# Performance work log

Measured on AMD Instinct MI355X. Metric: run time of the kernel, lower is better.

## Reference

```python
import jax, jax.numpy as jnp
import numpy as np

DT = 0.05
N_STEPS = 3
DAMP = 0.5
C2 = 1.0  # wave_speed^2


def _shift(u, k):
    # causal shift along T (axis=1): prepend k zeros, drop last k
    T = u.shape[1]
    return jnp.pad(u, ((0, 0), (k, 0), (0, 0)))[:, :T, :]


def dx(u):
    return u - _shift(u, 1)


def dxx(u):
    return u - 2.0 * _shift(u, 1) + _shift(u, 2)


def dxxx(u):
    return u - 3.0 * _shift(u, 1) + 3.0 * _shift(u, 2) - _shift(u, 3)


def dxxxx(u):
    return u - 4.0 * _shift(u, 1) + 6.0 * _shift(u, 2) - 4.0 * _shift(u, 3) + _shift(u, 4)


def _rk4_second_order(u0, rhs, dt, n_steps):
    # state (u, v), u_t = v, v_t = rhs(u, v); zero initial velocity
    u, v = u0, jnp.zeros_like(u0)
    for _ in range(n_steps):
        k1u, k1v = v, rhs(u, v)
        k2u, k2v = v + 0.5 * dt * k1v, rhs(u + 0.5 * dt * k1u, v + 0.5 * dt * k1v)
        k3u, k3v = v + 0.5 * dt * k2v, rhs(u + 0.5 * dt * k2u, v + 0.5 * dt * k2v)
        k4u, k4v = v + dt * k3v, rhs(u + dt * k3u, v + dt * k3v)
        u = u + (dt / 6.0) * (k1u + 2.0 * k2u + 2.0 * k3u + k4u)
        v = v + (dt / 6.0) * (k1v + 2.0 * k2v + 2.0 * k3v + k4v)
    return u


def _rk4_first_order(u0, rhs, dt, n_steps):
    u = u0
    for _ in range(n_steps):
        k1 = rhs(u)
        k2 = rhs(u + 0.5 * dt * k1)
        k3 = rhs(u + 0.5 * dt * k2)
        k4 = rhs(u + dt * k3)
        u = u + (dt / 6.0) * (k1 + 2.0 * k2 + 2.0 * k3 + k4)
    return u


def sine_gordon(u0):
    rhs = lambda u, v: C2 * dxx(u) - jnp.sin(u) - DAMP * v
    return _rk4_second_order(u0, rhs, DT, N_STEPS)


def kdv(u0):
    rhs = lambda u: -6.0 * u * dx(u) - dxxx(u) - DAMP * u
    return _rk4_first_order(u0, rhs, DT * 0.5, N_STEPS)


def heimburg_jackson(u0):
    rhs = lambda u, v: dx((1.0 + u + u * u) * dx(u)) - dxxxx(u) - DAMP * v
    return _rk4_second_order(u0, rhs, DT * 0.5, N_STEPS)


def setup_inputs() -> dict:
    key = jax.random.key(0)
    kx, kw = jax.random.split(key)
    B, T, D = 4, 4096, 1024
    x = jax.random.normal(kx, (B, T, D), dtype=jnp.float32)
    solver_mix = jnp.ones((3,), dtype=jnp.float32) / 3.0
    W = jax.random.normal(kw, (D, D), dtype=jnp.float32) * (1.0 / np.sqrt(D))
    b = jnp.zeros((D,), dtype=jnp.float32)
    return {"x": x, "solver_mix": solver_mix, "W": W, "b": b}


def reference(x, solver_mix, W, b):
    x_field = jnp.tanh(x) * 2.0
    w = jax.nn.softmax(solver_mix, axis=0)
    evolved = (
        w[0] * sine_gordon(x_field)
        + w[1] * kdv(x_field)
        + w[2] * heimburg_jackson(x_field)
    )
    out = jnp.einsum("btd,ed->bte", evolved, W) + b
    return out
```

## Files before the change

### kernel.cpp

```cpp
#include <hip/hip_runtime.h>
#include <hip/hip_bf16.h>


typedef __bf16 bf16x8 __attribute__((ext_vector_type(8)));
typedef __bf16 bf16x4 __attribute__((ext_vector_type(4)));
typedef float  floatx4 __attribute__((ext_vector_type(4)));

#define T_DIM 4096
#define D_DIM 1024
#define NP    16
#define HALO  48
#define NCH   32
#define TINT  (NCH * NP - HALO)
#define NTT   9

__device__ __forceinline__ float sg_rhs(float c, float m1, float m2, float vv) {
  float dxx = fmaf(-2.f, m1, c) + m2;
  return dxx - __sinf(c) - 0.5f * vv;
}
__device__ __forceinline__ float kdv_rhs(float c, float m1, float m2, float m3) {
  float dxu = c - m1;
  float dx3 = fmaf(-3.f, m1, c) + fmaf(3.f, m2, -m3);
  return fmaf(-6.f * c, dxu, -dx3 - 0.5f * c);
}
__device__ __forceinline__ float hj_rhs(float c, float m1, float m2, float m3,
                                        float m4, float vv) {
  float gi = (fmaf(c, c, c) + 1.f) * (c - m1);
  float gm = (fmaf(m1, m1, m1) + 1.f) * (m1 - m2);
  float d4 = fmaf(-4.f, m3, fmaf(6.f, m2, fmaf(-4.f, m1, c))) + m4;
  return (gi - gm) - d4 - 0.5f * vv;
}

#define AT(F, i) (((i) >= 0) ? F[(i)] : hl[4 + (i)])
#define XCHG(F) do { \
    hl[0] = __shfl_up(F[NP - 4], 1, 32); \
    hl[1] = __shfl_up(F[NP - 3], 1, 32); \
    hl[2] = __shfl_up(F[NP - 2], 1, 32); \
    hl[3] = __shfl_up(F[NP - 1], 1, 32); \
  } while (0)

__global__ __launch_bounds__(256, 2)
void pde_kernel(const float* __restrict__ x, const float* __restrict__ mix,
                __bf16* __restrict__ evout) {
  const int tid  = threadIdx.x;
  const int tr   = tid & 31;
  const int dcol = tid >> 5;
  const int yq   = blockIdx.y >> 3;
  const int yr   = blockIdx.y & 7;
  const int d    = (yr * 16 + yq) * 8 + dcol;
  const int b    = blockIdx.z;
  const int t0   = blockIdx.x * TINT;
  const int tb   = t0 - HALO + tr * NP;

  float s0 = mix[0], s1 = mix[1], s2 = mix[2];
  float mxv = fmaxf(s0, fmaxf(s1, s2));
  float e0 = __expf(s0 - mxv), e1 = __expf(s1 - mxv), e2 = __expf(s2 - mxv);
  float inv = 1.f / (e0 + e1 + e2);
  float w0 = e0 * inv, w1 = e1 * inv, w2 = e2 * inv;

  const float* xp = x + ((size_t)b * T_DIM) * D_DIM + d;

  float u0[NP], u[NP], v[NP], ut[NP], vt[NP], au[NP], av[NP], ev[NP], hl[4];

  #pragma unroll
  for (int j = 0; j < NP; ++j) {
    int t = tb + j;
    float xv = (t >= 0 && t < T_DIM) ? xp[(size_t)t * D_DIM] : 0.f;
    float xc = fminf(fmaxf(xv, -9.f), 9.f);
    float ex = __expf(2.f * xc);
    u0[j] = 2.f - 4.f * __builtin_amdgcn_rcpf(ex + 1.f);
  }

  {
    const float dt = 0.05f, h = 0.025f, w6 = dt * (1.f / 6.f);
    #pragma unroll
    for (int j = 0; j < NP; ++j) { u[j] = u0[j]; v[j] = 0.f; }
    #pragma unroll 1
    for (int s = 0; s < 3; ++s) {
      XCHG(u);
      #pragma unroll
      for (int i = NP - 1; i >= 0; --i) {
        float k = sg_rhs(u[i], AT(u, i - 1), AT(u, i - 2), v[i]);
        au[i] = v[i]; av[i] = k;
        ut[i] = fmaf(h, v[i], u[i]);
        vt[i] = fmaf(h, k, v[i]);
      }
      XCHG(ut);
      #pragma unroll
      for (int i = NP - 1; i >= 0; --i) {
        float k = sg_rhs(ut[i], AT(ut, i - 1), AT(ut, i - 2), vt[i]);
        au[i] = fmaf(2.f, vt[i], au[i]); av[i] = fmaf(2.f, k, av[i]);
        float nu = fmaf(h, vt[i], u[i]);
        vt[i] = fmaf(h, k, v[i]);
        ut[i] = nu;
      }
      XCHG(ut);
      #pragma unroll
      for (int i = NP - 1; i >= 0; --i) {
        float k = sg_rhs(ut[i], AT(ut, i - 1), AT(ut, i - 2), vt[i]);
        au[i] = fmaf(2.f, vt[i], au[i]); av[i] = fmaf(2.f, k, av[i]);
        float nu = fmaf(dt, vt[i], u[i]);
        vt[i] = fmaf(dt, k, v[i]);
        ut[i] = nu;
      }
      XCHG(ut);
      #pragma unroll
      for (int i = NP - 1; i >= 0; --i) {
        float k = sg_rhs(ut[i], AT(ut, i - 1), AT(ut, i - 2), vt[i]);
        au[i] += vt[i]; av[i] += k;
        u[i] = fmaf(w6, au[i], u[i]);
        v[i] = fmaf(w6, av[i], v[i]);
      }
    }
    #pragma unroll
    for (int j = 0; j < NP; ++j) ev[j] = w0 * u[j];
  }

  {
    const float dt = 0.025f, h = 0.0125f, w6 = dt * (1.f / 6.f);
    #pragma unroll
    for (int j = 0; j < NP; ++j) u[j] = u0[j];
    #pragma unroll 1
    for (int s = 0; s < 3; ++s) {
      XCHG(u);
      #pragma unroll
      for (int i = NP - 1; i >= 0; --i) {
        float k = kdv_rhs(u[i], AT(u, i - 1), AT(u, i - 2), AT(u, i - 3));
        au[i] = k;
        ut[i] = fmaf(h, k, u[i]);
      }
      XCHG(ut);
      #pragma unroll
      for (int i = NP - 1; i >= 0; --i) {
        float k = kdv_rhs(ut[i], AT(ut, i - 1), AT(ut, i - 2), AT(ut, i - 3));
        au[i] = fmaf(2.f, k, au[i]);
        ut[i] = fmaf(h, k, u[i]);
      }
      XCHG(ut);
      #pragma unroll
      for (int i = NP - 1; i >= 0; --i) {
        float k = kdv_rhs(ut[i], AT(ut, i - 1), AT(ut, i - 2), AT(ut, i - 3));
        au[i] = fmaf(2.f, k, au[i]);
        ut[i] = fmaf(dt, k, u[i]);
      }
      XCHG(ut);
      #pragma unroll
      for (int i = NP - 1; i >= 0; --i) {
        float k = kdv_rhs(ut[i], AT(ut, i - 1), AT(ut, i - 2), AT(ut, i - 3));
        u[i] = fmaf(w6, au[i] + k, u[i]);
      }
    }
    #pragma unroll
    for (int j = 0; j < NP; ++j) ev[j] = fmaf(w1, u[j], ev[j]);
  }

  {
    const float dt = 0.025f, h = 0.0125f, w6 = dt * (1.f / 6.f);
    #pragma unroll
    for (int j = 0; j < NP; ++j) { u[j] = u0[j]; v[j] = 0.f; }
    #pragma unroll 1
    for (int s = 0; s < 3; ++s) {
      XCHG(u);
      #pragma unroll
      for (int i = NP - 1; i >= 0; --i) {
        float k = hj_rhs(u[i], AT(u, i - 1), AT(u, i - 2), AT(u, i - 3),
                         AT(u, i - 4), v[i]);
        au[i] = v[i]; av[i] = k;
        ut[i] = fmaf(h, v[i], u[i]);
        vt[i] = fmaf(h, k, v[i]);
      }
      XCHG(ut);
      #pragma unroll
      for (int i = NP - 1; i >= 0; --i) {
        float k = hj_rhs(ut[i], AT(ut, i - 1), AT(ut, i - 2), AT(ut, i - 3),
                         AT(ut, i - 4), vt[i]);
        au[i] = fmaf(2.f, vt[i], au[i]); av[i] = fmaf(2.f, k, av[i]);
        float nu = fmaf(h, vt[i], u[i]);
        vt[i] = fmaf(h, k, v[i]);
        ut[i] = nu;
      }
      XCHG(ut);
      #pragma unroll
      for (int i = NP - 1; i >= 0; --i) {
        float k = hj_rhs(ut[i], AT(ut, i - 1), AT(ut, i - 2), AT(ut, i - 3),
                         AT(ut, i - 4), vt[i]);
        au[i] = fmaf(2.f, vt[i], au[i]); av[i] = fmaf(2.f, k, av[i]);
        float nu = fmaf(dt, vt[i], u[i]);
        vt[i] = fmaf(dt, k, v[i]);
        ut[i] = nu;
      }
      XCHG(ut);
      #pragma unroll
      for (int i = NP - 1; i >= 0; --i) {
        float k = hj_rhs(ut[i], AT(ut, i - 1), AT(ut, i - 2), AT(ut, i - 3),
                         AT(ut, i - 4), vt[i]);
        au[i] += vt[i]; av[i] += k;
        u[i] = fmaf(w6, au[i], u[i]);
        v[i] = fmaf(w6, av[i], v[i]);
      }
    }
    #pragma unroll
    for (int j = 0; j < NP; ++j) ev[j] = fmaf(w2, u[j], ev[j]);
  }

  if (tr >= 3) {
    #pragma unroll
    for (int j = 0; j < NP; ++j) {
      int t = tb + j;
      if (t < T_DIM)
        evout[((size_t)(b * T_DIM + t)) * D_DIM + d] = (__bf16)ev[j];
    }
  }
}

__global__ __launch_bounds__(256)
void convert_w(const float* __restrict__ W, __bf16* __restrict__ Wb) {
  int i = blockIdx.x * 256 + threadIdx.x;
  float4 f = ((const float4*)W)[i];
  bf16x4 o = {(__bf16)f.x, (__bf16)f.y, (__bf16)f.z, (__bf16)f.w};
  ((bf16x4*)Wb)[i] = o;
}

#define GK   1024

__global__ __launch_bounds__(512, 1)
void gemm_kernel(const __bf16* __restrict__ A, const __bf16* __restrict__ Bw,
                 const float* __restrict__ bias, float* __restrict__ out) {
  __shared__ __align__(16) __bf16 As[2][256 * 64];
  __shared__ __align__(16) __bf16 Bs[2][256 * 64];

  const int tid  = threadIdx.x;
  const int lane = tid & 63;
  const int wid  = tid >> 6;
  const int m0   = blockIdx.x * 256;
  const int n0   = blockIdx.y * 256;
  const int wm   = (wid >> 2) * 128;
  const int wn   = (wid & 3) * 64;
  const int l15  = lane & 15;
  const int quad = lane >> 4;

  const int sr  = lane >> 3;
  const int skc = (lane & 7) ^ sr;

  const __bf16* aBase = A  + (size_t)(m0 + wid * 32 + sr) * GK + skc * 8;
  const __bf16* bBase = Bw + (size_t)(n0 + wid * 32 + sr) * GK + skc * 8;

#define STAGE(buf, kt) do {                                                   \
    _Pragma("unroll")                                                         \
    for (int p = 0; p < 4; ++p)                                               \
      __builtin_amdgcn_global_load_lds(                                       \
          (const uint32_t*)(aBase + (size_t)(p * 8) * GK + (kt)),             \
          (uint32_t*)&As[buf][(wid * 32 + p * 8) * 64], 16, 0, 0);            \
    _Pragma("unroll")                                                         \
    for (int p = 0; p < 4; ++p)                                               \
      __builtin_amdgcn_global_load_lds(                                       \
          (const uint32_t*)(bBase + (size_t)(p * 8) * GK + (kt)),             \
          (uint32_t*)&Bs[buf][(wid * 32 + p * 8) * 64], 16, 0, 0);            \
  } while (0)

  floatx4 acc[8][4] = {};

  STAGE(0, 0);
  __syncthreads();

  int cur = 0;
  for (int kt = 64; kt <= GK; kt += 64) {
    if (kt < GK) STAGE(cur ^ 1, kt);
    const __bf16* as = As[cur];
    const __bf16* bs = Bs[cur];
    #pragma unroll
    for (int c = 0; c < 2; ++c) {
      bf16x8 af[8], bfr[4];
      int kcg = c * 4 + quad;
      #pragma unroll
      for (int i = 0; i < 8; ++i) {
        int ra = wm + i * 16 + l15;
        af[i] = *(const bf16x8*)(&as[ra * 64 + ((kcg ^ (ra & 7)) * 8)]);
      }
      #pragma unroll
      for (int j = 0; j < 4; ++j) {
        int rb = wn + j * 16 + l15;
        bfr[j] = *(const bf16x8*)(&bs[rb * 64 + ((kcg ^ (rb & 7)) * 8)]);
      }
      #pragma unroll
      for (int i = 0; i < 8; ++i)
        #pragma unroll
        for (int j = 0; j < 4; ++j)
          acc[i][j] = __builtin_amdgcn_mfma_f32_16x16x32_bf16(
              af[i], bfr[j], acc[i][j], 0, 0, 0);
    }
    __syncthreads();
    cur ^= 1;
  }
#undef STAGE

  #pragma unroll
  for (int j = 0; j < 4; ++j) {
    int n = n0 + wn + j * 16 + l15;
    float bv = bias[n];
    #pragma unroll
    for (int i = 0; i < 8; ++i) {
      int mb = m0 + wm + i * 16 + quad * 4;
      #pragma unroll
      for (int r = 0; r < 4; ++r)
        out[(size_t)(mb + r) * 1024 + n] = acc[i][j][r] + bv;
    }
  }
}

extern "C" void kernel_launch(void* const* d_in, const int* in_sizes, int n_in,
                              void* d_out, int out_size, void* d_ws, size_t ws_size,
                              hipStream_t stream) {
  const float* x    = (const float*)d_in[0];
  const float* mix  = (const float*)d_in[1];
  const float* W    = (const float*)d_in[2];
  const float* bias = (const float*)d_in[3];
  float* out = (float*)d_out;

  __bf16* ev = (__bf16*)d_ws;
  __bf16* Wb = (__bf16*)((char*)d_ws + (size_t)32 * 1024 * 1024);

  convert_w<<<dim3((D_DIM * D_DIM / 4) / 256), 256, 0, stream>>>(W, Wb);
  pde_kernel<<<dim3(NTT, 128, 4), 256, 0, stream>>>(x, mix, ev);
  gemm_kernel<<<dim3(16384 / 256, 1024 / 256), 512, 0, stream>>>(ev, Wb, bias, out);
}
```

Baseline: 324.4 us.

## Halve PDE per-thread points, reuse HJ flux terms, and hand-pipeline GEMM barriers

The PDE kernel now gives each thread 8 time points instead of 16 and spreads a column over a full 64-lane wavefront, with launch bounds raised to allow 4 blocks per CU. This lowers register pressure so occupancy can rise. The Heimburg-Jackson RHS now precomputes the nonlinear flux g once per point and reuses it for neighbours, removing the duplicate gm computation. The GEMM main loop is restructured with explicit vmcnt/lgkmcnt waits, raw s_barriers and a peeled final iteration, so the next tile's global-to-LDS loads can overlap compute. The d-column mapping also changes, which alters memory coalescing and access order.

```diff
diff --git a/kernel.cpp b/kernel.cpp
--- a/kernel.cpp
+++ b/kernel.cpp
@@ -8,9 +8,9 @@
 
 #define T_DIM 4096
 #define D_DIM 1024
-#define NP    16
+#define NP    8
 #define HALO  48
-#define NCH   32
+#define NCH   64
 #define TINT  (NCH * NP - HALO)
 #define NTT   9
 
@@ -23,31 +23,30 @@
   float dx3 = fmaf(-3.f, m1, c) + fmaf(3.f, m2, -m3);
   return fmaf(-6.f * c, dxu, -dx3 - 0.5f * c);
 }
-__device__ __forceinline__ float hj_rhs(float c, float m1, float m2, float m3,
-                                        float m4, float vv) {
-  float gi = (fmaf(c, c, c) + 1.f) * (c - m1);
-  float gm = (fmaf(m1, m1, m1) + 1.f) * (m1 - m2);
+__device__ __forceinline__ float hj_rhs2(float c, float m1, float m2, float m3,
+                                         float m4, float dg, float vv) {
   float d4 = fmaf(-4.f, m3, fmaf(6.f, m2, fmaf(-4.f, m1, c))) + m4;
-  return (gi - gm) - d4 - 0.5f * vv;
+  return (dg - d4) - 0.5f * vv;
+}
+__device__ __forceinline__ float hj_g(float c, float m1) {
+  return (fmaf(c, c, c) + 1.f) * (c - m1);
 }
 
 #define AT(F, i) (((i) >= 0) ? F[(i)] : hl[4 + (i)])
 #define XCHG(F) do { \
-    hl[0] = __shfl_up(F[NP - 4], 1, 32); \
-    hl[1] = __shfl_up(F[NP - 3], 1, 32); \
-    hl[2] = __shfl_up(F[NP - 2], 1, 32); \
-    hl[3] = __shfl_up(F[NP - 1], 1, 32); \
+    hl[0] = __shfl_up(F[NP - 4], 1, 64); \
+    hl[1] = __shfl_up(F[NP - 3], 1, 64); \
+    hl[2] = __shfl_up(F[NP - 2], 1, 64); \
+    hl[3] = __shfl_up(F[NP - 1], 1, 64); \
   } while (0)
 
-__global__ __launch_bounds__(256, 2)
+__global__ __launch_bounds__(256, 4)
 void pde_kernel(const float* __restrict__ x, const float* __restrict__ mix,
                 __bf16* __restrict__ evout) {
   const int tid  = threadIdx.x;
-  const int tr   = tid & 31;
-  const int dcol = tid >> 5;
-  const int yq   = blockIdx.y >> 3;
-  const int yr   = blockIdx.y & 7;
-  const int d    = (yr * 16 + yq) * 8 + dcol;
+  const int tr   = tid & 63;
+  const int dcol = tid >> 6;
+  const int d    = blockIdx.y * 4 + dcol;
   const int b    = blockIdx.z;
   const int t0   = blockIdx.x * TINT;
   const int tb   = t0 - HALO + tr * NP;
@@ -156,54 +155,69 @@
 
   {
     const float dt = 0.025f, h = 0.0125f, w6 = dt * (1.f / 6.f);
+    float g[NP], gB;
+#define HJ_GPRE(SRC) do {                                                  \
+      gB = hj_g(hl[3], hl[2]);                                             \
+      _Pragma("unroll")                                                    \
+      for (int i_ = 0; i_ < NP; ++i_)                                      \
+        g[i_] = hj_g(SRC[i_], AT(SRC, i_ - 1));                            \
+    } while (0)
+#define DG(i) ((i) ? (g[(i) - 1]) : gB)
+
     #pragma unroll
     for (int j = 0; j < NP; ++j) { u[j] = u0[j]; v[j] = 0.f; }
     #pragma unroll 1
     for (int s = 0; s < 3; ++s) {
       XCHG(u);
-      #pragma unroll
-      for (int i = NP - 1; i >= 0; --i) {
-        float k = hj_rhs(u[i], AT(u, i - 1), AT(u, i - 2), AT(u, i - 3),
-                         AT(u, i - 4), v[i]);
+      HJ_GPRE(u);
+      #pragma unroll
+      for (int i = NP - 1; i >= 0; --i) {
+        float k = hj_rhs2(u[i], AT(u, i - 1), AT(u, i - 2), AT(u, i - 3),
+                          AT(u, i - 4), g[i] - DG(i), v[i]);
         au[i] = v[i]; av[i] = k;
         ut[i] = fmaf(h, v[i], u[i]);
         vt[i] = fmaf(h, k, v[i]);
       }
       XCHG(ut);
-      #pragma unroll
-      for (int i = NP - 1; i >= 0; --i) {
-        float k = hj_rhs(ut[i], AT(ut, i - 1), AT(ut, i - 2), AT(ut, i - 3),
-                         AT(ut, i - 4), vt[i]);
+      HJ_GPRE(ut);
+      #pragma unroll
+      for (int i = NP - 1; i >= 0; --i) {
+        float k = hj_rhs2(ut[i], AT(ut, i - 1), AT(ut, i - 2), AT(ut, i - 3),
+                          AT(ut, i - 4), g[i] - DG(i), vt[i]);
         au[i] = fmaf(2.f, vt[i], au[i]); av[i] = fmaf(2.f, k, av[i]);
         float nu = fmaf(h, vt[i], u[i]);
         vt[i] = fmaf(h, k, v[i]);
         ut[i] = nu;
       }
       XCHG(ut);
-      #pragma unroll
-      for (int i = NP - 1; i >= 0; --i) {
-        float k = hj_rhs(ut[i], AT(ut, i - 1), AT(ut, i - 2), AT(ut, i - 3),
-                         AT(ut, i - 4), vt[i]);
+      HJ_GPRE(ut);
+      #pragma unroll
+      for (int i = NP - 1; i >= 0; --i) {
+        float k = hj_rhs2(ut[i], AT(ut, i - 1), AT(ut, i - 2), AT(ut, i - 3),
+                          AT(ut, i - 4), g[i] - DG(i), vt[i]);
         au[i] = fmaf(2.f, vt[i], au[i]); av[i] = fmaf(2.f, k, av[i]);
         float nu = fmaf(dt, vt[i], u[i]);
         vt[i] = fmaf(dt, k, v[i]);
         ut[i] = nu;
       }
       XCHG(ut);
-      #pragma unroll
-      for (int i = NP - 1; i >= 0; --i) {
-        float k = hj_rhs(ut[i], AT(ut, i - 1), AT(ut, i - 2), AT(ut, i - 3),
-                         AT(ut, i - 4), vt[i]);
+      HJ_GPRE(ut);
+      #pragma unroll
+      for (int i = NP - 1; i >= 0; --i) {
+        float k = hj_rhs2(ut[i], AT(ut, i - 1), AT(ut, i - 2), AT(ut, i - 3),
+                          AT(ut, i - 4), g[i] - DG(i), vt[i]);
         au[i] += vt[i]; av[i] += k;
         u[i] = fmaf(w6, au[i], u[i]);
         v[i] = fmaf(w6, av[i], v[i]);
       }
     }
+#undef HJ_GPRE
+#undef DG
     #pragma unroll
     for (int j = 0; j < NP; ++j) ev[j] = fmaf(w2, u[j], ev[j]);
   }
 
-  if (tr >= 3) {
+  if (tr >= HALO / NP) {
     #pragma unroll
     for (int j = 0; j < NP; ++j) {
       int t = tb + j;
@@ -258,41 +272,56 @@
           (uint32_t*)&Bs[buf][(wid * 32 + p * 8) * 64], 16, 0, 0);            \
   } while (0)
 
+#define COMPUTE(buf) do {                                                     \
+    const __bf16* as_ = As[buf];                                              \
+    const __bf16* bs_ = Bs[buf];                                              \
+    _Pragma("unroll")                                                         \
+    for (int c = 0; c < 2; ++c) {                        \
+      bf16x8 af[8], bfr[4];                                                   \
+      int kcg = c * 4 + quad;                  \
+      _Pragma("unroll")                                                       \
+      for (int i = 0; i < 8; ++i) {                                           \
+        int ra = wm + i * 16 + l15;                                           \
+        af[i] = *(const bf16x8*)(&as_[ra * 64 + ((kcg ^ (ra & 7)) * 8)]);     \
+      }                                                                       \
+      _Pragma("unroll")                                                       \
+      for (int j = 0; j < 4; ++j) {                                           \
+        int rb = wn + j * 16 + l15;                                           \
+        bfr[j] = *(const bf16x8*)(&bs_[rb * 64 + ((kcg ^ (rb & 7)) * 8)]);    \
+      }                                                                       \
+      _Pragma("unroll")                                                       \
+      for (int i = 0; i < 8; ++i)                                             \
+        _Pragma("unroll")                                                     \
+        for (int j = 0; j < 4; ++j)                                           \
+          acc[i][j] = __builtin_amdgcn_mfma_f32_16x16x32_bf16(                \
+              af[i], bfr[j], acc[i][j], 0, 0, 0);                             \
+    }                                                                         \
+  } while (0)
+
   floatx4 acc[8][4] = {};
 
   STAGE(0, 0);
-  __syncthreads();
-
   int cur = 0;
-  for (int kt = 64; kt <= GK; kt += 64) {
-    if (kt < GK) STAGE(cur ^ 1, kt);
-    const __bf16* as = As[cur];
-    const __bf16* bs = Bs[cur];
-    #pragma unroll
-    for (int c = 0; c < 2; ++c) {
-      bf16x8 af[8], bfr[4];
-      int kcg = c * 4 + quad;
-      #pragma unroll
-      for (int i = 0; i < 8; ++i) {
-        int ra = wm + i * 16 + l15;
-        af[i] = *(const bf16x8*)(&as[ra * 64 + ((kcg ^ (ra & 7)) * 8)]);
-      }
-      #pragma unroll
-      for (int j = 0; j < 4; ++j) {
-        int rb = wn + j * 16 + l15;
-        bfr[j] = *(const bf16x8*)(&bs[rb * 64 + ((kcg ^ (rb & 7)) * 8)]);
-      }
-      #pragma unroll
-      for (int i = 0; i < 8; ++i)
-        #pragma unroll
-        for (int j = 0; j < 4; ++j)
-          acc[i][j] = __builtin_amdgcn_mfma_f32_16x16x32_bf16(
-              af[i], bfr[j], acc[i][j], 0, 0, 0);
-    }
-    __syncthreads();
+  for (int kt = 64; kt < GK; kt += 64) {
+    STAGE(cur ^ 1, kt);
+    asm volatile("s_waitcnt vmcnt(8)" ::: "memory");
+    __builtin_amdgcn_sched_barrier(0);
+    __builtin_amdgcn_s_barrier();
+    __builtin_amdgcn_sched_barrier(0);
+    COMPUTE(cur);
+    asm volatile("s_waitcnt lgkmcnt(0)" ::: "memory");
+    __builtin_amdgcn_sched_barrier(0);
+    __builtin_amdgcn_s_barrier();
+    __builtin_amdgcn_sched_barrier(0);
     cur ^= 1;
   }
+  asm volatile("s_waitcnt vmcnt(0)" ::: "memory");
+  __builtin_amdgcn_sched_barrier(0);
+  __builtin_amdgcn_s_barrier();
+  __builtin_amdgcn_sched_barrier(0);
+  COMPUTE(cur);
 #undef STAGE
+#undef COMPUTE
 
   #pragma unroll
   for (int j = 0; j < 4; ++j) {
@@ -321,6 +350,6 @@
   __bf16* Wb = (__bf16*)((char*)d_ws + (size_t)32 * 1024 * 1024);
 
   convert_w<<<dim3((D_DIM * D_DIM / 4) / 256), 256, 0, stream>>>(W, Wb);
-  pde_kernel<<<dim3(NTT, 128, 4), 256, 0, stream>>>(x, mix, ev);
+  pde_kernel<<<dim3(NTT, D_DIM / 4, 4), 256, 0, stream>>>(x, mix, ev);
   gemm_kernel<<<dim3(16384 / 256, 1024 / 256), 512, 0, stream>>>(ev, Wb, bias, out);
 }
```

After: 323.2 us. Within noise of the previous version (-0.4%).
